# Kernel optimization log

Measured on AMD Instinct MI355X. Metric: run time of the kernel, lower is better.

Reference implementation:

```python
import jax, jax.numpy as jnp
import numpy as np
import math

B, S, H, D = 1, 2048, 12, 128
DIM = H * D
BLKQ, BLKK = 128, 64
TOPK = 0.2
EPS = 1e-6
NEG = -1e30


def setup_inputs() -> dict:
    key = jax.random.key(0)
    ks = jax.random.split(key, 8)
    hidden_states = jax.random.normal(ks[0], (B, S, DIM), jnp.float32)
    # interleaved RoPE tables: even slots hold cos, odd slots hold sin phase copies
    pos = np.arange(S, dtype=np.float64)[:, None]
    inv = 1.0 / (10000.0 ** (np.arange(0, D, 2, dtype=np.float64) / D))
    ang = pos * inv[None, :]                       # [S, D/2]
    freqs_cos = jnp.asarray(np.repeat(np.cos(ang), 2, axis=-1), jnp.float32).reshape(1, S, 1, D)
    freqs_sin = jnp.asarray(np.repeat(np.sin(ang), 2, axis=-1), jnp.float32).reshape(1, S, 1, D)
    sc = 1.0 / math.sqrt(DIM)
    Wq = jax.random.normal(ks[1], (DIM, DIM), jnp.float32) * sc
    Wk = jax.random.normal(ks[2], (DIM, DIM), jnp.float32) * sc
    Wv = jax.random.normal(ks[3], (DIM, DIM), jnp.float32) * sc
    Wo = jax.random.normal(ks[4], (DIM, DIM), jnp.float32) * sc
    bq = jax.random.normal(ks[5], (DIM,), jnp.float32) * 0.01
    bk = jax.random.normal(ks[6], (DIM,), jnp.float32) * 0.01
    bv = jax.random.normal(ks[7], (DIM,), jnp.float32) * 0.01
    bo = jnp.zeros((DIM,), jnp.float32)
    gq = jnp.ones((DIM,), jnp.float32)
    gk = jnp.ones((DIM,), jnp.float32)
    return dict(hidden_states=hidden_states, freqs_cos=freqs_cos, freqs_sin=freqs_sin,
                Wq=Wq, bq=bq, Wk=Wk, bk=bk, Wv=Wv, bv=bv, Wo=Wo, bo=bo, gq=gq, gk=gk)


def _rmsnorm(x, g):
    return x * jax.lax.rsqrt(jnp.mean(x * x, axis=-1, keepdims=True) + EPS) * g


def _rope(x, fc, fs):
    # x: [B,S,H,D]; interleaved even/odd rotation as in _apply_rotary_emb
    x1 = x[..., 0::2]
    x2 = x[..., 1::2]
    cos = fc[..., 0::2]
    sin = fs[..., 1::2]
    even = x1 * cos - x2 * sin
    odd = x1 * sin + x2 * cos
    return jnp.stack([even, odd], axis=-1).reshape(x.shape)


def _sla(q, k, v):
    # q,k,v: [B,H,S,D]. Top-k block-sparse exact attention + linear attention
    # (softmax feature map) on the unselected blocks, jointly normalized.
    nqb, nkb = S // BLKQ, S // BLKK
    ksel = max(1, int(math.ceil(TOPK * nkb)))
    qb = q.reshape(B, H, nqb, BLKQ, D).mean(axis=3)
    kb = k.reshape(B, H, nkb, BLKK, D).mean(axis=3)
    blk_scores = jnp.einsum('bhqd,bhkd->bhqk', qb, kb)
    _, idx = jax.lax.top_k(blk_scores, ksel)                  # [B,H,nqb,ksel]
    bmask = (jax.nn.one_hot(idx, nkb, dtype=jnp.float32).sum(axis=-2) > 0)
    mask = jnp.repeat(jnp.repeat(bmask, BLKQ, axis=2), BLKK, axis=3)  # [B,H,S,S]

    scale = 1.0 / math.sqrt(D)
    s = jnp.einsum('bhqd,bhkd->bhqk', q, k) * scale
    m = jnp.max(jnp.where(mask, s, NEG), axis=-1, keepdims=True)
    p = jnp.where(mask, jnp.exp(s - m), 0.0)
    num_s = jnp.einsum('bhqk,bhkd->bhqd', p, v)
    den_s = p.sum(axis=-1, keepdims=True)

    lq = jax.nn.softmax(q, axis=-1)
    lk = jax.nn.softmax(k, axis=-1)
    L = jnp.where(mask, 0.0, jnp.einsum('bhqd,bhkd->bhqk', lq, lk))
    num_l = jnp.einsum('bhqk,bhkd->bhqd', L, v)
    den_l = L.sum(axis=-1, keepdims=True)

    w = jnp.exp(-m)  # bring linear part onto the max-shifted exp scale
    return (num_s + w * num_l) / (den_s + w * den_l)


def reference(hidden_states, freqs_cos, freqs_sin, Wq, bq, Wk, bk, Wv, bv, Wo, bo, gq, gk):
    q = _rmsnorm(hidden_states @ Wq + bq, gq).reshape(B, S, H, D)
    k = _rmsnorm(hidden_states @ Wk + bk, gk).reshape(B, S, H, D)
    v = (hidden_states @ Wv + bv).reshape(B, S, H, D)
    q = _rope(q, freqs_cos, freqs_sin)
    k = _rope(k, freqs_cos, freqs_sin)
    q, k, v = (t.transpose(0, 2, 1, 3) for t in (q, k, v))  # [B,H,S,D]
    o = _sla(q, k, v)
    o = o.transpose(0, 2, 1, 3).reshape(B, S, DIM)
    return o @ Wo + bo
```

## Files before the change

### kernel.cpp

```cpp
#include <hip/hip_runtime.h>
#include <hip/hip_bf16.h>

#define SQ   2048
#define DIMM 1536
#define QS   4608
#define NH   12
#define DH   128
#define NQB  16
#define NKB  32
#define KSEL 7

typedef unsigned short u16;
typedef __bf16 bf16x8 __attribute__((ext_vector_type(8)));
typedef _Float16 f16x8 __attribute__((ext_vector_type(8)));
typedef short  s16x8  __attribute__((ext_vector_type(8)));
typedef float  f32x4  __attribute__((ext_vector_type(4)));

__device__ __forceinline__ float bf2f(u16 u) {
  unsigned int x = ((unsigned int)u) << 16;
  return __builtin_bit_cast(float, x);
}
__device__ __forceinline__ u16 f2bf(float f) {
  unsigned int x = __builtin_bit_cast(unsigned int, f);
  x += 0x7fffu + ((x >> 16) & 1u);
  return (u16)(x >> 16);
}

typedef __attribute__((address_space(3))) void lds_vt;
typedef const __attribute__((address_space(1))) void g_vt;
__device__ __forceinline__ void dma16(const void* g, void* l) {
  __builtin_amdgcn_global_load_lds((g_vt*)g, (lds_vt*)l, 16, 0, 0);
}

__global__ __launch_bounds__(256) void prep_hs(const float* __restrict__ hs,
                                               u16* __restrict__ hh,
                                               u16* __restrict__ hl) {
  size_t i = ((size_t)blockIdx.x * 256 + threadIdx.x) * 8;
  f32x4 a = *(const f32x4*)&hs[i];
  f32x4 b = *(const f32x4*)&hs[i + 4];
  s16x8 h, l;
  #pragma unroll
  for (int j = 0; j < 4; j++) {
    u16 hj = f2bf(a[j]); h[j] = (short)hj; l[j] = (short)f2bf(a[j] - bf2f(hj));
    u16 hk = f2bf(b[j]); h[4 + j] = (short)hk; l[4 + j] = (short)f2bf(b[j] - bf2f(hk));
  }
  *(s16x8*)&hh[i] = h;
  *(s16x8*)&hl[i] = l;
}

__global__ __launch_bounds__(256) void prep_w(const float* __restrict__ W0,
                                              const float* __restrict__ W1,
                                              const float* __restrict__ W2,
                                              const float* __restrict__ W3,
                                              u16* __restrict__ WTh,
                                              u16* __restrict__ WTl) {
  __shared__ float tile[64][65];
  int wi = blockIdx.z;
  const float* W = (wi == 0) ? W0 : (wi == 1) ? W1 : (wi == 2) ? W2 : W3;
  int x = threadIdx.x & 63, y = threadIdx.x >> 6;
  int k0 = blockIdx.y * 64, n0 = blockIdx.x * 64;
  #pragma unroll
  for (int i = 0; i < 16; i++) {
    int k = y + i * 4;
    tile[k][x] = W[(size_t)(k0 + k) * DIMM + n0 + x];
  }
  __syncthreads();
  size_t obase = (size_t)wi * DIMM * DIMM;
  #pragma unroll
  for (int i = 0; i < 16; i++) {
    int n = y + i * 4;
    float v = tile[x][n];
    size_t oi = obase + (size_t)(n0 + n) * DIMM + k0 + x;
    if (wi == 3) {
      WTh[oi] = __builtin_bit_cast(u16, (_Float16)v);
    } else {
      u16 h = f2bf(v);
      WTh[oi] = h;
      WTl[oi] = f2bf(v - bf2f(h));
    }
  }
}

__global__ __launch_bounds__(256) void gemm3_k(const u16* __restrict__ Ahp,
                                               const u16* __restrict__ Alp,
                                               const u16* __restrict__ WTh,
                                               const u16* __restrict__ WTl,
                                               const float* __restrict__ bq,
                                               const float* __restrict__ bk,
                                               const float* __restrict__ bv,
                                               float* __restrict__ C) {
  __shared__ u16 As[2][128][64];
  __shared__ u16 Bs[2][128][64];
  const int tid = threadIdx.x;
  const int w = tid >> 6, lane = tid & 63, quad = lane >> 4, l16 = lane & 15;
  const int wr = w >> 1, wc = w & 1;
  const int m_base = blockIdx.y * 128;
  const int nt = blockIdx.x;
  const int wi = nt / 12;
  const int n_in = (nt % 12) * 128;
  const u16* Bh0 = WTh + ((size_t)wi * DIMM + n_in) * DIMM;
  const u16* Bl0 = WTl + ((size_t)wi * DIMM + n_in) * DIMM;
  const float* bias = (wi == 0) ? bq : (wi == 1) ? bk : bv;
  const bool split = (wi != 2);

  const int srow = lane >> 3;
  const int skc = (((lane & 7) ^ srow) * 8);
  const int rx = (l16 & 7);

  f32x4 zero4 = {0.f, 0.f, 0.f, 0.f};
  f32x4 acc[4][4];
  #pragma unroll
  for (int i = 0; i < 4; i++)
    #pragma unroll
    for (int j = 0; j < 4; j++) acc[i][j] = zero4;

  for (int k0 = 0; k0 < DIMM; k0 += 64) {
    #pragma unroll
    for (int c = 0; c < 4; c++) {
      int r0 = w * 32 + c * 8;
      int row = r0 + srow;
      dma16(&Ahp[(size_t)(m_base + row) * DIMM + k0 + skc], &As[0][r0][0]);
      dma16(&Bh0[(size_t)row * DIMM + k0 + skc], &Bs[0][r0][0]);
      if (split) {
        dma16(&Alp[(size_t)(m_base + row) * DIMM + k0 + skc], &As[1][r0][0]);
        dma16(&Bl0[(size_t)row * DIMM + k0 + skc], &Bs[1][r0][0]);
      }
    }
    __syncthreads();
    #pragma unroll
    for (int kk = 0; kk < 2; kk++) {
      const int coff = ((kk * 4 + quad) ^ rx) * 8;
      bf16x8 afh[4], afl[4], bfh[4], bfl[4];
      #pragma unroll
      for (int i = 0; i < 4; i++)
        afh[i] = __builtin_bit_cast(bf16x8,
                 *(const s16x8*)&As[0][wr * 64 + i * 16 + l16][coff]);
      #pragma unroll
      for (int j = 0; j < 4; j++)
        bfh[j] = __builtin_bit_cast(bf16x8,
                 *(const s16x8*)&Bs[0][wc * 64 + j * 16 + l16][coff]);
      if (split) {
        #pragma unroll
        for (int i = 0; i < 4; i++)
          afl[i] = __builtin_bit_cast(bf16x8,
                   *(const s16x8*)&As[1][wr * 64 + i * 16 + l16][coff]);
        #pragma unroll
        for (int j = 0; j < 4; j++)
          bfl[j] = __builtin_bit_cast(bf16x8,
                   *(const s16x8*)&Bs[1][wc * 64 + j * 16 + l16][coff]);
      }
      #pragma unroll
      for (int i = 0; i < 4; i++)
        #pragma unroll
        for (int j = 0; j < 4; j++) {
          acc[i][j] = __builtin_amdgcn_mfma_f32_16x16x32_bf16(afh[i], bfh[j], acc[i][j], 0, 0, 0);
          if (split) {
            acc[i][j] = __builtin_amdgcn_mfma_f32_16x16x32_bf16(afh[i], bfl[j], acc[i][j], 0, 0, 0);
            acc[i][j] = __builtin_amdgcn_mfma_f32_16x16x32_bf16(afl[i], bfh[j], acc[i][j], 0, 0, 0);
          }
        }
    }
    __syncthreads();
  }
  #pragma unroll
  for (int i = 0; i < 4; i++)
    #pragma unroll
    for (int j = 0; j < 4; j++) {
      int tc = wc * 64 + j * 16 + l16;
      float bv2 = bias[n_in + tc];
      #pragma unroll
      for (int rg = 0; rg < 4; rg++) {
        int r = m_base + wr * 64 + i * 16 + quad * 4 + rg;
        C[(size_t)r * QS + nt * 128 + tc] = acc[i][j][rg] + bv2;
      }
    }
}

__global__ __launch_bounds__(256) void gemm_o(const u16* __restrict__ Ap,
                                              const u16* __restrict__ Bp,
                                              const float* __restrict__ bias,
                                              float* __restrict__ C) {
  __shared__ u16 As[64][64];
  __shared__ u16 Bs[128][64];
  const int tid = threadIdx.x;
  const int w = tid >> 6, lane = tid & 63, quad = lane >> 4, l16 = lane & 15;
  const int wr = w >> 1, wc = w & 1;
  const int m_base = blockIdx.y * 64, n_base = blockIdx.x * 128;
  const int srow = lane >> 3;
  const int skc = (((lane & 7) ^ srow) * 8);
  const int rx = (l16 & 7);

  f32x4 zero4 = {0.f, 0.f, 0.f, 0.f};
  f32x4 acc[2][4];
  #pragma unroll
  for (int i = 0; i < 2; i++)
    #pragma unroll
    for (int j = 0; j < 4; j++) acc[i][j] = zero4;

  for (int k0 = 0; k0 < DIMM; k0 += 64) {
    #pragma unroll
    for (int c = 0; c < 2; c++) {
      int r0 = w * 16 + c * 8;
      int row = r0 + srow;
      dma16(&Ap[(size_t)(m_base + row) * DIMM + k0 + skc], &As[r0][0]);
    }
    #pragma unroll
    for (int c = 0; c < 4; c++) {
      int r0 = w * 32 + c * 8;
      int row = r0 + srow;
      dma16(&Bp[(size_t)(n_base + row) * DIMM + k0 + skc], &Bs[r0][0]);
    }
    __syncthreads();
    #pragma unroll
    for (int kk = 0; kk < 2; kk++) {
      const int coff = ((kk * 4 + quad) ^ rx) * 8;
      f16x8 af[2], bf[4];
      #pragma unroll
      for (int i = 0; i < 2; i++)
        af[i] = __builtin_bit_cast(f16x8,
                *(const s16x8*)&As[wr * 32 + i * 16 + l16][coff]);
      #pragma unroll
      for (int j = 0; j < 4; j++)
        bf[j] = __builtin_bit_cast(f16x8,
                *(const s16x8*)&Bs[wc * 64 + j * 16 + l16][coff]);
      #pragma unroll
      for (int i = 0; i < 2; i++)
        #pragma unroll
        for (int j = 0; j < 4; j++)
          acc[i][j] = __builtin_amdgcn_mfma_f32_16x16x32_f16(af[i], bf[j], acc[i][j], 0, 0, 0);
    }
    __syncthreads();
  }
  #pragma unroll
  for (int i = 0; i < 2; i++)
    #pragma unroll
    for (int j = 0; j < 4; j++) {
      int c = n_base + wc * 64 + j * 16 + l16;
      float bv2 = bias[c];
      #pragma unroll
      for (int rg = 0; rg < 4; rg++) {
        int r = m_base + wr * 32 + i * 16 + quad * 4 + rg;
        C[(size_t)r * DIMM + c] = acc[i][j][rg] + bv2;
      }
    }
}

__global__ __launch_bounds__(256) void norm_rope_k(float* __restrict__ qkv,
                                                   const float* __restrict__ gq,
                                                   const float* __restrict__ gk,
                                                   const float* __restrict__ fc,
                                                   const float* __restrict__ fs,
                                                   u16* __restrict__ qbf,
                                                   u16* __restrict__ kbf) {
  int s = blockIdx.x;
  float* row = qkv + (size_t)s * QS + (blockIdx.y == 0 ? 0 : DIMM);
  const float* g = (blockIdx.y == 0) ? gq : gk;
  u16* obase = (blockIdx.y == 0) ? qbf : kbf;
  int t = threadIdx.x;
  float ss = 0.f;
  #pragma unroll
  for (int i = 0; i < 6; i++) {
    float v = row[t + i * 256];
    ss += v * v;
  }
  #pragma unroll
  for (int m = 1; m < 64; m <<= 1) ss += __shfl_xor(ss, m, 64);
  __shared__ float wsum[4];
  if ((t & 63) == 0) wsum[t >> 6] = ss;
  __syncthreads();
  float tot = wsum[0] + wsum[1] + wsum[2] + wsum[3];
  float sc = rsqrtf(tot / 1536.0f + 1e-6f);
  #pragma unroll
  for (int i = 0; i < 3; i++) {
    int p = t + i * 256;
    int h = p >> 6, ip = p & 63;
    int base = h * 128 + 2 * ip;
    float x1 = row[base] * sc * g[base];
    float x2 = row[base + 1] * sc * g[base + 1];
    float c = fc[(size_t)s * 128 + 2 * ip];
    float sn = fs[(size_t)s * 128 + 2 * ip + 1];
    float ev = x1 * c - x2 * sn;
    float od = x1 * sn + x2 * c;
    row[base]     = ev;
    row[base + 1] = od;
    int gsk = ip >> 2, e = (2 * ip) & 7;
    int cc = (gsk & 8) | ((gsk ^ (s & 7)) & 7);
    u16* ob = obase + ((size_t)h * SQ + s) * 128;
    unsigned int pack = (unsigned int)f2bf(ev) | ((unsigned int)f2bf(od) << 16);
    *(unsigned int*)&ob[cc * 8 + e] = pack;
  }
}

__global__ __launch_bounds__(256) void prep_vT(const float* __restrict__ vf,
                                               u16* __restrict__ vbfT) {
  __shared__ float vt[64][132];
  int b = blockIdx.x, h = blockIdx.y, tid = threadIdx.x;
  #pragma unroll
  for (int i = 0; i < 8; i++) {
    int idx = i * 256 + tid; int key = idx >> 5, d4 = (idx & 31) * 4;
    *(f32x4*)&vt[key][d4] = *(const f32x4*)&vf[(size_t)(b * 64 + key) * QS + h * DH + d4];
  }
  __syncthreads();
  u16* out = vbfT + ((size_t)(h * NKB + b)) * 128 * 64;
  #pragma unroll
  for (int i = 0; i < 4; i++) {
    int idx = i * 256 + tid;
    int d = idx >> 3, c = idx & 7;
    int g = c ^ (d & 7);
    s16x8 o;
    #pragma unroll
    for (int e = 0; e < 8; e++) o[e] = (short)f2bf(vt[g * 8 + e][d]);
    *(s16x8*)&out[d * 64 + c * 8] = o;
  }
}

__global__ __launch_bounds__(128) void means_k(const float* __restrict__ qf,
                                               const float* __restrict__ kf,
                                               float* __restrict__ qb,
                                               float* __restrict__ kb) {
  int h = blockIdx.y, t = threadIdx.x;
  if (blockIdx.x < NQB) {
    int qi = blockIdx.x;
    float a = 0.f;
    for (int r = 0; r < 128; r++) a += qf[(size_t)(qi * 128 + r) * QS + h * DH + t];
    qb[(h * NQB + qi) * DH + t] = a * (1.0f / 128.0f);
  } else {
    int ki = blockIdx.x - NQB;
    float a = 0.f;
    for (int r = 0; r < 64; r++) a += kf[(size_t)(ki * 64 + r) * QS + h * DH + t];
    kb[(h * NKB + ki) * DH + t] = a * (1.0f / 64.0f);
  }
}

__global__ __launch_bounds__(64) void topk_k(const float* __restrict__ qb,
                                             const float* __restrict__ kb,
                                             int* __restrict__ sel) {
  int h = blockIdx.y, qi = blockIdx.x, t = threadIdx.x;
  __shared__ float scs[NKB];
  if (t < NKB) {
    float a = 0.f;
    for (int d = 0; d < DH; d++)
      a += qb[(h * NQB + qi) * DH + d] * kb[(h * NKB + t) * DH + d];
    scs[t] = a;
  }
  __syncthreads();
  if (t == 0) {
    unsigned int used = 0;
    for (int it = 0; it < KSEL; it++) {
      float best = -3.4e38f; int bi = 0;
      for (int j = 0; j < NKB; j++)
        if (!((used >> j) & 1) && scs[j] > best) { best = scs[j]; bi = j; }
      used |= 1u << bi;
      sel[(h * NQB + qi) * 8 + it] = bi;
    }
  }
}

__global__ __launch_bounds__(256) void kv_k(const float* __restrict__ kf,
                                            const float* __restrict__ vf,
                                            float* __restrict__ KV,
                                            float* __restrict__ slk) {
  int h = blockIdx.y, kb = blockIdx.x, t = threadIdx.x;
  __shared__ float lkt[64][132];
  __shared__ float vt[64][132];
  #pragma unroll
  for (int i = 0; i < 8; i++) {
    int idx = i * 256 + t; int r = idx >> 5, d4 = (idx & 31) * 4;
    *(f32x4*)&vt[r][d4] = *(const f32x4*)&vf[(size_t)(kb * 64 + r) * QS + h * DH + d4];
  }
  {
    int r = t >> 2, q4 = t & 3;
    const float* kr = kf + (size_t)(kb * 64 + r) * QS + h * DH;
    f32x4 x[8];
    float mx = -3.4e38f;
    #pragma unroll
    for (int i = 0; i < 8; i++) {
      x[i] = *(const f32x4*)&kr[q4 * 32 + i * 4];
      mx = fmaxf(mx, fmaxf(fmaxf(x[i][0], x[i][1]), fmaxf(x[i][2], x[i][3])));
    }
    mx = fmaxf(mx, __shfl_xor(mx, 1, 64));
    mx = fmaxf(mx, __shfl_xor(mx, 2, 64));
    float sum = 0.f;
    #pragma unroll
    for (int i = 0; i < 8; i++) {
      #pragma unroll
      for (int e = 0; e < 4; e++) { float v = __expf(x[i][e] - mx); x[i][e] = v; sum += v; }
    }
    sum += __shfl_xor(sum, 1, 64);
    sum += __shfl_xor(sum, 2, 64);
    float inv = 1.0f / sum;
    #pragma unroll
    for (int i = 0; i < 8; i++) {
      x[i] *= inv;
      *(f32x4*)&lkt[r][q4 * 32 + i * 4] = x[i];
    }
  }
  __syncthreads();
  int d1 = t >> 1, hf = t & 1;
  f32x4 a[16];
  f32x4 zero4 = {0.f, 0.f, 0.f, 0.f};
  #pragma unroll
  for (int i = 0; i < 16; i++) a[i] = zero4;
  for (int j = 0; j < 64; j++) {
    float lv = lkt[j][d1];
    #pragma unroll
    for (int q = 0; q < 16; q++) {
      f32x4 vv = *(const f32x4*)&vt[j][hf * 64 + q * 4];
      a[q] += lv * vv;
    }
  }
  float* out = KV + ((size_t)(h * NKB + kb) * DH + d1) * DH + hf * 64;
  #pragma unroll
  for (int q = 0; q < 16; q++) *(f32x4*)&out[q * 4] = a[q];
  if (t < 128) {
    float s2 = 0.f;
    for (int j = 0; j < 64; j++) s2 += lkt[j][t];
    slk[(h * NKB + kb) * DH + t] = s2;
  }
}

__global__ __launch_bounds__(256) void kvtot_k(const float* __restrict__ KV,
                                               const float* __restrict__ slk,
                                               float* __restrict__ KVtot,
                                               float* __restrict__ sltot) {
  int h = blockIdx.y; int e = blockIdx.x * 256 + threadIdx.x;
  float a = 0.f;
  for (int b = 0; b < NKB; b++) a += KV[(size_t)(h * NKB + b) * 16384 + e];
  KVtot[(size_t)h * 16384 + e] = a;
  if (blockIdx.x == 0 && threadIdx.x < 128) {
    float s2 = 0.f;
    for (int b = 0; b < NKB; b++) s2 += slk[(h * NKB + b) * DH + threadIdx.x];
    sltot[h * DH + threadIdx.x] = s2;
  }
}

__global__ __launch_bounds__(256) void attn_k(const u16* __restrict__ qbf,
                                              const u16* __restrict__ kbf,
                                              const u16* __restrict__ vbfT,
                                              const int* __restrict__ sel,
                                              const float* __restrict__ KV,
                                              const float* __restrict__ slk,
                                              const float* __restrict__ KVtot,
                                              const float* __restrict__ sltot,
                                              u16* __restrict__ of16) {
  __shared__ u16 smem[25600];
  __shared__ float mrow[64], lrow[64], dent[64], slsh[128];
  __shared__ int selsh[KSEL];
  u16* qt  = smem;
  u16* vtT = smem + 8192;
  u16* kt  = smem + 16384;
  u16* ptb = smem + 16384;
  u16* MT  = smem + 8192;

  int h = blockIdx.y, qi = blockIdx.x, tid = threadIdx.x;
  int w = tid >> 6, lane = tid & 63, quad = lane >> 4, l16 = lane & 15;

  {
    const u16* qsrc = qbf + ((size_t)h * SQ + qi * 64) * 128;
    #pragma unroll
    for (int c = 0; c < 4; c++)
      dma16(qsrc + (w * 16 + c * 4) * 128 + lane * 8, &qt[(w * 16 + c * 4) * 128]);
  }
  if (tid < KSEL) selsh[tid] = sel[(h * NQB + (qi >> 1)) * 8 + tid];
  __syncthreads();

  float m_run[4], l_run[4];
  f32x4 zero4 = {0.f, 0.f, 0.f, 0.f};
  f32x4 oacc[8];
  #pragma unroll
  for (int rg = 0; rg < 4; rg++) { m_run[rg] = -3.0e38f; l_run[rg] = 0.f; }
  #pragma unroll
  for (int nt = 0; nt < 8; nt++) oacc[nt] = zero4;

  for (int bi = 0; bi < KSEL; bi++) {
    int b = selsh[bi];
    {
      const u16* ksrc = kbf + ((size_t)h * SQ + b * 64) * 128;
      #pragma unroll
      for (int c = 0; c < 4; c++)
        dma16(ksrc + (w * 16 + c * 4) * 128 + lane * 8, &kt[(w * 16 + c * 4) * 128]);
      const u16* vsrc = vbfT + ((size_t)(h * NKB + b)) * 128 * 64;
      #pragma unroll
      for (int c = 0; c < 4; c++)
        dma16(vsrc + (w * 32 + c * 8) * 64 + lane * 8, &vtT[(w * 32 + c * 8) * 64]);
    }
    __syncthreads();

    f32x4 sacc[4];
    #pragma unroll
    for (int nt = 0; nt < 4; nt++) sacc[nt] = zero4;
    __builtin_amdgcn_s_setprio(1);
    #pragma unroll
    for (int kk = 0; kk < 4; kk++) {
      const int kkq = kk * 4 + quad;
      const int qoff = ((kkq & 8) | ((kkq ^ (l16 & 7)) & 7)) * 8;
      bf16x8 af = __builtin_bit_cast(bf16x8, *(const s16x8*)&qt[(w * 16 + l16) * 128 + qoff]);
      #pragma unroll
      for (int nt = 0; nt < 4; nt++) {
        bf16x8 bfr = __builtin_bit_cast(bf16x8, *(const s16x8*)&kt[(nt * 16 + l16) * 128 + qoff]);
        sacc[nt] = __builtin_amdgcn_mfma_f32_16x16x32_bf16(af, bfr, sacc[nt], 0, 0, 0);
      }
    }
    __builtin_amdgcn_s_setprio(0);
    const float SCALE = 0.08838834764831845f;
    #pragma unroll
    for (int nt = 0; nt < 4; nt++) sacc[nt] *= SCALE;

    #pragma unroll
    for (int rg = 0; rg < 4; rg++) {
      float bmax = fmaxf(fmaxf(sacc[0][rg], sacc[1][rg]),
                         fmaxf(sacc[2][rg], sacc[3][rg]));
      bmax = fmaxf(bmax, __shfl_xor(bmax, 1, 64));
      bmax = fmaxf(bmax, __shfl_xor(bmax, 2, 64));
      bmax = fmaxf(bmax, __shfl_xor(bmax, 4, 64));
      bmax = fmaxf(bmax, __shfl_xor(bmax, 8, 64));
      float mold = m_run[rg];
      float mnew = fmaxf(mold, bmax);
      float alpha = __expf(mold - mnew);
      float rs = 0.f;
      #pragma unroll
      for (int nt = 0; nt < 4; nt++) {
        float p = __expf(sacc[nt][rg] - mnew);
        sacc[nt][rg] = p; rs += p;
      }
      rs += __shfl_xor(rs, 1, 64);
      rs += __shfl_xor(rs, 2, 64);
      rs += __shfl_xor(rs, 4, 64);
      rs += __shfl_xor(rs, 8, 64);
      m_run[rg] = mnew;
      l_run[rg] = l_run[rg] * alpha + rs;
      #pragma unroll
      for (int nt = 0; nt < 8; nt++) oacc[nt][rg] *= alpha;
    }
    __syncthreads();
    #pragma unroll
    for (int rg = 0; rg < 4; rg++) {
      int r = w * 16 + quad * 4 + rg;
      #pragma unroll
      for (int nt = 0; nt < 4; nt++) ptb[r * 72 + nt * 16 + l16] = f2bf(sacc[nt][rg]);
    }
    __syncthreads();

    __builtin_amdgcn_s_setprio(1);
    #pragma unroll
    for (int kk = 0; kk < 2; kk++) {
      bf16x8 pa = __builtin_bit_cast(bf16x8, *(const s16x8*)&ptb[(w * 16 + l16) * 72 + kk * 32 + quad * 8]);
      #pragma unroll
      for (int nt = 0; nt < 8; nt++) {
        const int voff = ((kk * 4 + quad) ^ (l16 & 7)) * 8;
        bf16x8 vb = __builtin_bit_cast(bf16x8, *(const s16x8*)&vtT[(nt * 16 + l16) * 64 + voff]);
        oacc[nt] = __builtin_amdgcn_mfma_f32_16x16x32_bf16(pa, vb, oacc[nt], 0, 0, 0);
      }
    }
    __builtin_amdgcn_s_setprio(0);
    __syncthreads();
  }

  if (l16 == 0) {
    #pragma unroll
    for (int rg = 0; rg < 4; rg++) {
      int r = w * 16 + quad * 4 + rg;
      mrow[r] = m_run[rg];
      lrow[r] = l_run[rg];
    }
  }
  if (tid < 128) {
    float a = sltot[h * DH + tid];
    #pragma unroll
    for (int i = 0; i < KSEL; i++) a -= slk[(h * NKB + selsh[i]) * DH + tid];
    slsh[tid] = a;
  }
  for (int i = 0; i < 16; i++) {
    int idx = i * 256 + tid;
    int e4 = idx * 4;
    int d1 = e4 >> 7, d2 = e4 & 127;
    f32x4 a = *(const f32x4*)&KVtot[(size_t)h * 16384 + e4];
    #pragma unroll
    for (int k2 = 0; k2 < KSEL; k2++) {
      f32x4 s4 = *(const f32x4*)&KV[(size_t)(h * NKB + selsh[k2]) * 16384 + e4];
      a -= s4;
    }
    #pragma unroll
    for (int j = 0; j < 4; j++) MT[(d2 + j) * 136 + d1] = f2bf(a[j]);
  }
  __syncthreads();

  {
    int r = tid >> 2, sub = tid & 3;
    float w_r = __expf(-mrow[r]);
    float mx = -3.4e38f;
    #pragma unroll
    for (int gi = 0; gi < 4; gi++) {
      int gc = sub * 4 + gi;
      int c = (gc & 8) | ((gc ^ (r & 7)) & 7);
      #pragma unroll
      for (int e = 0; e < 8; e++) mx = fmaxf(mx, bf2f(qt[r * 128 + c * 8 + e]));
    }
    mx = fmaxf(mx, __shfl_xor(mx, 1, 64));
    mx = fmaxf(mx, __shfl_xor(mx, 2, 64));
    float sum = 0.f;
    #pragma unroll
    for (int gi = 0; gi < 4; gi++) {
      int gc = sub * 4 + gi;
      int c = (gc & 8) | ((gc ^ (r & 7)) & 7);
      #pragma unroll
      for (int e = 0; e < 8; e++) sum += __expf(bf2f(qt[r * 128 + c * 8 + e]) - mx);
    }
    sum += __shfl_xor(sum, 1, 64);
    sum += __shfl_xor(sum, 2, 64);
    float sc2 = w_r / sum;
    float dl = 0.f;
    #pragma unroll
    for (int gi = 0; gi < 4; gi++) {
      int gc = sub * 4 + gi;
      int c = (gc & 8) | ((gc ^ (r & 7)) & 7);
      #pragma unroll
      for (int e = 0; e < 8; e++) {
        float lq = __expf(bf2f(qt[r * 128 + c * 8 + e]) - mx) * sc2;
        dl += lq * slsh[gc * 8 + e];
        qt[r * 128 + c * 8 + e] = f2bf(lq);
      }
    }
    dl += __shfl_xor(dl, 1, 64);
    dl += __shfl_xor(dl, 2, 64);
    if (sub == 0) dent[r] = lrow[r] + dl;
  }
  __syncthreads();

  __builtin_amdgcn_s_setprio(1);
  #pragma unroll
  for (int kk = 0; kk < 4; kk++) {
    const int kkq = kk * 4 + quad;
    const int qoff = ((kkq & 8) | ((kkq ^ (l16 & 7)) & 7)) * 8;
    bf16x8 af = __builtin_bit_cast(bf16x8, *(const s16x8*)&qt[(w * 16 + l16) * 128 + qoff]);
    #pragma unroll
    for (int nt = 0; nt < 8; nt++) {
      bf16x8 mb = __builtin_bit_cast(bf16x8, *(const s16x8*)&MT[(nt * 16 + l16) * 136 + kk * 32 + quad * 8]);
      oacc[nt] = __builtin_amdgcn_mfma_f32_16x16x32_bf16(af, mb, oacc[nt], 0, 0, 0);
    }
  }
  __builtin_amdgcn_s_setprio(0);

  #pragma unroll
  for (int rg = 0; rg < 4; rg++) {
    int r = w * 16 + quad * 4 + rg;
    float inv = 1.0f / dent[r];
    #pragma unroll
    for (int nt = 0; nt < 8; nt++) {
      int c = nt * 16 + l16;
      float v = oacc[nt][rg] * inv;
      size_t oi = (size_t)(qi * 64 + r) * DIMM + h * DH + c;
      of16[oi] = __builtin_bit_cast(u16, (_Float16)v);
    }
  }
}

extern "C" void kernel_launch(void* const* d_in, const int* in_sizes, int n_in,
                              void* d_out, int out_size, void* d_ws, size_t ws_size,
                              hipStream_t stream) {
  const float* hs = (const float*)d_in[0];
  const float* fc = (const float*)d_in[1];
  const float* fs = (const float*)d_in[2];
  const float* Wq = (const float*)d_in[3];
  const float* bq = (const float*)d_in[4];
  const float* Wk = (const float*)d_in[5];
  const float* bk = (const float*)d_in[6];
  const float* Wv = (const float*)d_in[7];
  const float* bv = (const float*)d_in[8];
  const float* Wo = (const float*)d_in[9];
  const float* bo = (const float*)d_in[10];
  const float* gq = (const float*)d_in[11];
  const float* gk = (const float*)d_in[12];

  char* p = (char*)d_ws;
  auto alloc = [&](size_t bytes) {
    char* r = p; p += (bytes + 255) & ~(size_t)255; return r;
  };
  u16* WTh = (u16*)alloc((size_t)4 * DIMM * DIMM * 2);
  u16* WTl = (u16*)alloc((size_t)4 * DIMM * DIMM * 2);
  u16* hsh = (u16*)alloc((size_t)SQ * DIMM * 2);
  u16* hsl = (u16*)alloc((size_t)SQ * DIMM * 2);
  float* qkv = (float*)alloc((size_t)SQ * QS * 4);
  u16* qbf = (u16*)alloc((size_t)NH * SQ * DH * 2);
  u16* kbf = (u16*)alloc((size_t)NH * SQ * DH * 2);
  u16* vbfT = (u16*)alloc((size_t)NH * NKB * DH * 64 * 2);
  float* qb = (float*)alloc((size_t)NH * NQB * DH * 4);
  float* kb = (float*)alloc((size_t)NH * NKB * DH * 4);
  int* sel = (int*)alloc((size_t)NH * NQB * 8 * 4);
  float* KV = (float*)alloc((size_t)NH * NKB * DH * DH * 4);
  float* slk = (float*)alloc((size_t)NH * NKB * DH * 4);
  float* KVtot = (float*)alloc((size_t)NH * DH * DH * 4);
  float* sltot = (float*)alloc((size_t)NH * DH * 4);

  float* qf = qkv;
  float* kf = qkv + DIMM;
  float* vf = qkv + 2 * DIMM;

  prep_hs<<<SQ * DIMM / (256 * 8), 256, 0, stream>>>(hs, hsh, hsl);
  prep_w<<<dim3(24, 24, 4), 256, 0, stream>>>(Wq, Wk, Wv, Wo, WTh, WTl);

  gemm3_k<<<dim3(36, 16), 256, 0, stream>>>(hsh, hsl, WTh, WTl, bq, bk, bv, qkv);

  norm_rope_k<<<dim3(SQ, 2), 256, 0, stream>>>(qkv, gq, gk, fc, fs, qbf, kbf);
  means_k<<<dim3(NQB + NKB, NH), 128, 0, stream>>>(qf, kf, qb, kb);
  topk_k<<<dim3(NQB, NH), 64, 0, stream>>>(qb, kb, sel);
  kv_k<<<dim3(NKB, NH), 256, 0, stream>>>(kf, vf, KV, slk);
  kvtot_k<<<dim3(64, NH), 256, 0, stream>>>(KV, slk, KVtot, sltot);
  prep_vT<<<dim3(NKB, NH), 256, 0, stream>>>(vf, vbfT);

  u16* of16 = hsh;
  attn_k<<<dim3(2 * NQB, NH), 256, 0, stream>>>(qbf, kbf, vbfT, sel, KV, slk, KVtot, sltot, of16);

  const u16* WTo = WTh + (size_t)3 * DIMM * DIMM;
  gemm_o<<<dim3(12, 32), 256, 0, stream>>>(of16, WTo, bo, (float*)d_out);
}
```

Measured before the change: 349.8 us.

## Halve QKV GEMM N-tile and move linear-attention KV build onto bf16 MFMA

The fused QKV GEMM now uses 128x64 tiles instead of 128x128, doubling the grid from 576 to 1152 blocks so more CUs stay busy. Separately, the per-block linear-attention K^T V product is moved from scalar fp32 FMAs to bf16 MFMA. It reuses the transposed bf16 V buffer, so prep_vT is launched before kv_k. The softmaxed K features are rounded to bf16, which lowers KV accuracy, and the smaller GEMM tile reduces data reuse per block.

```diff
diff --git a/kernel.cpp b/kernel.cpp
--- a/kernel.cpp
+++ b/kernel.cpp
@@ -90,14 +90,13 @@
                                                const float* __restrict__ bv,
                                                float* __restrict__ C) {
   __shared__ u16 As[2][128][64];
-  __shared__ u16 Bs[2][128][64];
+  __shared__ u16 Bs[2][64][64];
   const int tid = threadIdx.x;
   const int w = tid >> 6, lane = tid & 63, quad = lane >> 4, l16 = lane & 15;
-  const int wr = w >> 1, wc = w & 1;
   const int m_base = blockIdx.y * 128;
   const int nt = blockIdx.x;
-  const int wi = nt / 12;
-  const int n_in = (nt % 12) * 128;
+  const int wi = nt / 24;
+  const int n_in = (nt % 24) * 64;
   const u16* Bh0 = WTh + ((size_t)wi * DIMM + n_in) * DIMM;
   const u16* Bl0 = WTl + ((size_t)wi * DIMM + n_in) * DIMM;
   const float* bias = (wi == 0) ? bq : (wi == 1) ? bk : bv;
@@ -108,9 +107,9 @@
   const int rx = (l16 & 7);
 
   f32x4 zero4 = {0.f, 0.f, 0.f, 0.f};
-  f32x4 acc[4][4];
-  #pragma unroll
-  for (int i = 0; i < 4; i++)
+  f32x4 acc[2][4];
+  #pragma unroll
+  for (int i = 0; i < 2; i++)
     #pragma unroll
     for (int j = 0; j < 4; j++) acc[i][j] = zero4;
 
@@ -120,37 +119,42 @@
       int r0 = w * 32 + c * 8;
       int row = r0 + srow;
       dma16(&Ahp[(size_t)(m_base + row) * DIMM + k0 + skc], &As[0][r0][0]);
+      if (split)
+        dma16(&Alp[(size_t)(m_base + row) * DIMM + k0 + skc], &As[1][r0][0]);
+    }
+    #pragma unroll
+    for (int c = 0; c < 2; c++) {
+      int r0 = w * 16 + c * 8;
+      int row = r0 + srow;
       dma16(&Bh0[(size_t)row * DIMM + k0 + skc], &Bs[0][r0][0]);
-      if (split) {
-        dma16(&Alp[(size_t)(m_base + row) * DIMM + k0 + skc], &As[1][r0][0]);
+      if (split)
         dma16(&Bl0[(size_t)row * DIMM + k0 + skc], &Bs[1][r0][0]);
-      }
     }
     __syncthreads();
     #pragma unroll
     for (int kk = 0; kk < 2; kk++) {
       const int coff = ((kk * 4 + quad) ^ rx) * 8;
-      bf16x8 afh[4], afl[4], bfh[4], bfl[4];
-      #pragma unroll
-      for (int i = 0; i < 4; i++)
+      bf16x8 afh[2], afl[2], bfh[4], bfl[4];
+      #pragma unroll
+      for (int i = 0; i < 2; i++)
         afh[i] = __builtin_bit_cast(bf16x8,
-                 *(const s16x8*)&As[0][wr * 64 + i * 16 + l16][coff]);
+                 *(const s16x8*)&As[0][w * 32 + i * 16 + l16][coff]);
       #pragma unroll
       for (int j = 0; j < 4; j++)
         bfh[j] = __builtin_bit_cast(bf16x8,
-                 *(const s16x8*)&Bs[0][wc * 64 + j * 16 + l16][coff]);
+                 *(const s16x8*)&Bs[0][j * 16 + l16][coff]);
       if (split) {
         #pragma unroll
-        for (int i = 0; i < 4; i++)
+        for (int i = 0; i < 2; i++)
           afl[i] = __builtin_bit_cast(bf16x8,
-                   *(const s16x8*)&As[1][wr * 64 + i * 16 + l16][coff]);
+                   *(const s16x8*)&As[1][w * 32 + i * 16 + l16][coff]);
         #pragma unroll
         for (int j = 0; j < 4; j++)
           bfl[j] = __builtin_bit_cast(bf16x8,
-                   *(const s16x8*)&Bs[1][wc * 64 + j * 16 + l16][coff]);
+                   *(const s16x8*)&Bs[1][j * 16 + l16][coff]);
       }
       #pragma unroll
-      for (int i = 0; i < 4; i++)
+      for (int i = 0; i < 2; i++)
         #pragma unroll
         for (int j = 0; j < 4; j++) {
           acc[i][j] = __builtin_amdgcn_mfma_f32_16x16x32_bf16(afh[i], bfh[j], acc[i][j], 0, 0, 0);
@@ -163,15 +167,15 @@
     __syncthreads();
   }
   #pragma unroll
-  for (int i = 0; i < 4; i++)
+  for (int i = 0; i < 2; i++)
     #pragma unroll
     for (int j = 0; j < 4; j++) {
-      int tc = wc * 64 + j * 16 + l16;
+      int tc = j * 16 + l16;
       float bv2 = bias[n_in + tc];
       #pragma unroll
       for (int rg = 0; rg < 4; rg++) {
-        int r = m_base + wr * 64 + i * 16 + quad * 4 + rg;
-        C[(size_t)r * QS + nt * 128 + tc] = acc[i][j][rg] + bv2;
+        int r = m_base + w * 32 + i * 16 + quad * 4 + rg;
+        C[(size_t)r * QS + nt * 64 + tc] = acc[i][j][rg] + bv2;
       }
     }
 }
@@ -357,16 +361,19 @@
 }
 
 __global__ __launch_bounds__(256) void kv_k(const float* __restrict__ kf,
-                                            const float* __restrict__ vf,
+                                            const u16* __restrict__ vbfT,
                                             float* __restrict__ KV,
                                             float* __restrict__ slk) {
+  __shared__ u16 lkT[128 * 72];
+  __shared__ u16 vtT[128 * 64];
   int h = blockIdx.y, kb = blockIdx.x, t = threadIdx.x;
-  __shared__ float lkt[64][132];
-  __shared__ float vt[64][132];
-  #pragma unroll
-  for (int i = 0; i < 8; i++) {
-    int idx = i * 256 + t; int r = idx >> 5, d4 = (idx & 31) * 4;
-    *(f32x4*)&vt[r][d4] = *(const f32x4*)&vf[(size_t)(kb * 64 + r) * QS + h * DH + d4];
+  int w = t >> 6, lane = t & 63, quad = lane >> 4, l16 = lane & 15;
+
+  {
+    const u16* vsrc = vbfT + ((size_t)(h * NKB + kb)) * 128 * 64;
+    #pragma unroll
+    for (int c = 0; c < 4; c++)
+      dma16(vsrc + (w * 32 + c * 8) * 64 + lane * 8, &vtT[(w * 32 + c * 8) * 64]);
   }
   {
     int r = t >> 2, q4 = t & 3;
@@ -382,40 +389,63 @@
     mx = fmaxf(mx, __shfl_xor(mx, 2, 64));
     float sum = 0.f;
     #pragma unroll
-    for (int i = 0; i < 8; i++) {
+    for (int i = 0; i < 8; i++)
       #pragma unroll
       for (int e = 0; e < 4; e++) { float v = __expf(x[i][e] - mx); x[i][e] = v; sum += v; }
-    }
     sum += __shfl_xor(sum, 1, 64);
     sum += __shfl_xor(sum, 2, 64);
     float inv = 1.0f / sum;
     #pragma unroll
-    for (int i = 0; i < 8; i++) {
-      x[i] *= inv;
-      *(f32x4*)&lkt[r][q4 * 32 + i * 4] = x[i];
-    }
+    for (int i = 0; i < 8; i++)
+      #pragma unroll
+      for (int e = 0; e < 4; e++)
+        lkT[(q4 * 32 + i * 4 + e) * 72 + r] = f2bf(x[i][e] * inv);
   }
   __syncthreads();
-  int d1 = t >> 1, hf = t & 1;
-  f32x4 a[16];
+
   f32x4 zero4 = {0.f, 0.f, 0.f, 0.f};
-  #pragma unroll
-  for (int i = 0; i < 16; i++) a[i] = zero4;
-  for (int j = 0; j < 64; j++) {
-    float lv = lkt[j][d1];
-    #pragma unroll
-    for (int q = 0; q < 16; q++) {
-      f32x4 vv = *(const f32x4*)&vt[j][hf * 64 + q * 4];
-      a[q] += lv * vv;
-    }
-  }
-  float* out = KV + ((size_t)(h * NKB + kb) * DH + d1) * DH + hf * 64;
-  #pragma unroll
-  for (int q = 0; q < 16; q++) *(f32x4*)&out[q * 4] = a[q];
+  f32x4 acc[2][8];
+  #pragma unroll
+  for (int i = 0; i < 2; i++)
+    #pragma unroll
+    for (int j = 0; j < 8; j++) acc[i][j] = zero4;
+  #pragma unroll
+  for (int kk = 0; kk < 2; kk++) {
+    bf16x8 af[2];
+    #pragma unroll
+    for (int i = 0; i < 2; i++)
+      af[i] = __builtin_bit_cast(bf16x8,
+              *(const s16x8*)&lkT[(w * 32 + i * 16 + l16) * 72 + kk * 32 + quad * 8]);
+    const int voff = ((kk * 4 + quad) ^ (l16 & 7)) * 8;
+    #pragma unroll
+    for (int j = 0; j < 8; j++) {
+      bf16x8 vb = __builtin_bit_cast(bf16x8, *(const s16x8*)&vtT[(j * 16 + l16) * 64 + voff]);
+      #pragma unroll
+      for (int i = 0; i < 2; i++)
+        acc[i][j] = __builtin_amdgcn_mfma_f32_16x16x32_bf16(af[i], vb, acc[i][j], 0, 0, 0);
+    }
+  }
+  float* out = KV + (size_t)(h * NKB + kb) * 16384;
+  #pragma unroll
+  for (int i = 0; i < 2; i++)
+    #pragma unroll
+    for (int j = 0; j < 8; j++) {
+      #pragma unroll
+      for (int rg = 0; rg < 4; rg++) {
+        int r = w * 32 + i * 16 + quad * 4 + rg;
+        int c = j * 16 + l16;
+        out[(size_t)r * 128 + c] = acc[i][j][rg];
+      }
+    }
   if (t < 128) {
-    float s2 = 0.f;
-    for (int j = 0; j < 64; j++) s2 += lkt[j][t];
-    slk[(h * NKB + kb) * DH + t] = s2;
+    float a = 0.f;
+    #pragma unroll
+    for (int c8 = 0; c8 < 8; c8++) {
+      s16x8 v8 = *(const s16x8*)&lkT[t * 72 + c8 * 8];
+      #pragma unroll
+      for (int e = 0; e < 8; e++) a += bf2f((u16)v8[e]);
+    }
+    slk[(h * NKB + kb) * DH + t] = a;
   }
 }
 
@@ -699,14 +729,14 @@
   prep_hs<<<SQ * DIMM / (256 * 8), 256, 0, stream>>>(hs, hsh, hsl);
   prep_w<<<dim3(24, 24, 4), 256, 0, stream>>>(Wq, Wk, Wv, Wo, WTh, WTl);
 
-  gemm3_k<<<dim3(36, 16), 256, 0, stream>>>(hsh, hsl, WTh, WTl, bq, bk, bv, qkv);
+  gemm3_k<<<dim3(72, 16), 256, 0, stream>>>(hsh, hsl, WTh, WTl, bq, bk, bv, qkv);
 
   norm_rope_k<<<dim3(SQ, 2), 256, 0, stream>>>(qkv, gq, gk, fc, fs, qbf, kbf);
+  prep_vT<<<dim3(NKB, NH), 256, 0, stream>>>(vf, vbfT);
   means_k<<<dim3(NQB + NKB, NH), 128, 0, stream>>>(qf, kf, qb, kb);
   topk_k<<<dim3(NQB, NH), 64, 0, stream>>>(qb, kb, sel);
-  kv_k<<<dim3(NKB, NH), 256, 0, stream>>>(kf, vf, KV, slk);
+  kv_k<<<dim3(NKB, NH), 256, 0, stream>>>(kf, vbfT, KV, slk);
   kvtot_k<<<dim3(64, NH), 256, 0, stream>>>(KV, slk, KVtot, sltot);
-  prep_vT<<<dim3(NKB, NH), 256, 0, stream>>>(vf, vbfT);
 
   u16* of16 = hsh;
   attn_k<<<dim3(2 * NQB, NH), 256, 0, stream>>>(qbf, kbf, vbfT, sel, KV, slk, KVtot, sltot, of16);
```

Result: faster. 307.8 us (-12.0%).
